# Kernel optimization log

Measured on AMD Instinct MI355X. Metric: run time of the kernel, lower is better.

## Reference

```python
import jax, jax.numpy as jnp
import numpy as np

B, M, H, E, V, U = 1024, 15, 256, 256, 30000, 1000


def setup_inputs() -> dict:
    key = jax.random.key(0)
    ks = jax.random.split(key, 24)
    s = 0.05  # weight init scale
    return {
        "input_ids": jax.random.randint(ks[0], (B, 1), 0, V),
        "input_embedding": jax.random.normal(ks[1], (B, 1, E), jnp.float32),
        "hidden": jax.random.normal(ks[2], (1, B, H), jnp.float32),
        "inter_output": jax.random.normal(ks[3], (B, M, H), jnp.float32),
        "user_list": jax.random.randint(ks[4], (B,), 0, U),
        # per-user parameter tables (torch ModuleLists of Linear); stored [in,out]
        "inter_W": jax.random.normal(ks[5], (U, H, H), jnp.float32) * s,
        "inter_b": jax.random.normal(ks[6], (U, H), jnp.float32) * s,
        "hidden_W": jax.random.normal(ks[7], (U, H, H), jnp.float32) * s,
        "hidden_b": jax.random.normal(ks[8], (U, H), jnp.float32) * s,
        "lt1_W": jax.random.normal(ks[9], (U, 2 * H, H), jnp.float32) * s,
        "lt1_b": jax.random.normal(ks[10], (U, H), jnp.float32) * s,
        "scale_W": jax.random.normal(ks[11], (U, H), jnp.float32) * s,
        "scale_b": jax.random.normal(ks[12], (U,), jnp.float32) * s,
        # GRU (1 layer), torch layout: W_ih [3H, 2E], W_hh [3H, H], gate order r,z,n
        "gru_Wih": jax.random.normal(ks[13], (3 * H, 2 * E), jnp.float32) * s,
        "gru_Whh": jax.random.normal(ks[14], (3 * H, H), jnp.float32) * s,
        "gru_bih": jax.random.normal(ks[15], (3 * H,), jnp.float32) * s,
        "gru_bhh": jax.random.normal(ks[16], (3 * H,), jnp.float32) * s,
        # output projection, stored [H, V]
        "lin_W": jax.random.normal(ks[17], (H, V), jnp.float32) * s,
        "lin_b": jax.random.normal(ks[18], (V,), jnp.float32) * s,
    }


def reference(input_ids, input_embedding, hidden, inter_output, user_list,
              inter_W, inter_b, hidden_W, hidden_b, lt1_W, lt1_b,
              scale_W, scale_b, gru_Wih, gru_Whh, gru_bih, gru_bhh,
              lin_W, lin_b):
    embedded_input = input_embedding  # dropout p=0 (eval)
    hidden_t = jnp.transpose(hidden, (1, 0, 2))  # [B,1,H]

    # per-user intra attention: gather user weights, batched GEMMs (replaces python loop)
    Wi = inter_W[user_list]                      # [B,H,H]
    inter_output_a = jnp.einsum('bmh,bho->bmo', inter_output, Wi) + inter_b[user_list][:, None, :]
    Wh = hidden_W[user_list]                     # [B,H,H]
    hidden_t_a = jnp.einsum('bih,bho->bio', hidden_t, Wh) + hidden_b[user_list][:, None, :]  # [B,1,H]
    cat = jnp.concatenate([jnp.broadcast_to(hidden_t_a, (hidden_t_a.shape[0], M, H)), inter_output_a], axis=2)  # [B,M,2H]
    result = jnp.tanh(jnp.einsum('bmk,bko->bmo', cat, lt1_W[user_list]) + lt1_b[user_list][:, None, :])  # [B,M,H]
    energies = jnp.einsum('bmh,bh->bm', result, scale_W[user_list]) + scale_b[user_list][:, None]  # [B,M]

    attn_weights = jax.nn.softmax(energies, axis=1)                      # [B,M]
    context = jnp.einsum('bm,bmh->bh', attn_weights, inter_output)[:, None, :]  # [B,1,H]

    gru_input = jnp.concatenate([embedded_input, context], axis=2)  # [B,1,2E]
    x = gru_input[:, 0, :]
    h = hidden[0]
    gi = x @ gru_Wih.T + gru_bih   # [B,3H]
    gh = h @ gru_Whh.T + gru_bhh
    gi_r, gi_z, gi_n = jnp.split(gi, 3, axis=1)
    gh_r, gh_z, gh_n = jnp.split(gh, 3, axis=1)
    r = jax.nn.sigmoid(gi_r + gh_r)
    z = jax.nn.sigmoid(gi_z + gh_z)
    n = jnp.tanh(gi_n + r * gh_n)
    h_new = (1.0 - z) * n + z * h
    gru_output = h_new[:, None, :]       # [B,1,H]
    hidden_new = h_new[None, :, :]       # [1,B,H]

    output = gru_output @ lin_W + lin_b  # [B,1,V]
    return (output, hidden_new, embedded_input, gru_output, attn_weights)
```

## Files before the change

### kernel.cpp

```cpp
#include <hip/hip_runtime.h>
#include <math.h>

#define B 1024
#define M 15
#define H 256
#define E 256
#define V 30000
#define U 1000

typedef float  vf4    __attribute__((ext_vector_type(4)));
typedef __bf16 bf16x8 __attribute__((ext_vector_type(8)));
typedef float  f32x4  __attribute__((ext_vector_type(4)));

#define O_OUT   0
#define O_HID   ((size_t)B*V)
#define O_EMB   (O_HID + (size_t)B*H)
#define O_GRU   (O_EMB + (size_t)B*E)
#define O_ATT   (O_GRU + (size_t)B*H)

#define GLDS(g, l) __builtin_amdgcn_global_load_lds( \
    (const __attribute__((address_space(1))) void*)(g), \
    (__attribute__((address_space(3))) void*)(l), 16, 0, 0)

union BF8 { __bf16 h[8]; bf16x8 v; };
union BF4 { __bf16 h[4]; unsigned long long u; };

__global__ __launch_bounds__(1024) void sort_kernel(
    const int* __restrict__ ul, int* __restrict__ order, int* __restrict__ rbase_g)
{
    __shared__ int cnt[1024];
    __shared__ int base[1024];
    const int tid = threadIdx.x;
    cnt[tid] = 0;
    __syncthreads();
    const int u = ul[tid];
    atomicAdd(&cnt[u], 1);
    __syncthreads();
    int c0 = cnt[tid];
    int v  = c0;
    for (int off = 1; off < 1024; off <<= 1) {
        int add = (tid >= off) ? cnt[tid - off] : 0;
        __syncthreads();
        v += add;
        cnt[tid] = v;
        __syncthreads();
    }
    base[tid]   = v - c0;
    rbase_g[tid] = v - c0;
    __syncthreads();
    int pos = atomicAdd(&base[u], 1);
    order[pos] = tid;
}

#define FB_ATTN 1024
#define FB_TR   500
#define FB_WC   256
#define FB_TOT  (FB_ATTN + FB_TR + FB_WC)

__global__ __launch_bounds__(256, 3) void fused_pre_kernel(
    const float* __restrict__ hidden,
    const float* __restrict__ inter_output,
    const int*   __restrict__ user_list,
    const int*   __restrict__ order,
    const int*   __restrict__ rbase,
    const float* __restrict__ inter_W,
    const float* __restrict__ inter_b,
    const float* __restrict__ hidden_W,
    const float* __restrict__ hidden_b,
    const float* __restrict__ lt1_W,
    const float* __restrict__ lt1_b,
    const float* __restrict__ scale_W,
    const float* __restrict__ scale_b,
    const float* __restrict__ emb,
    const float* __restrict__ Wih,
    const float* __restrict__ Whh,
    const float* __restrict__ lin_W,
    float* __restrict__ out,
    __bf16* __restrict__ xcat,
    __bf16* __restrict__ wcat,
    __bf16* __restrict__ WT)
{
    __shared__ __align__(16) char smem[34432];
    const int bid = blockIdx.x;
    const int tid = threadIdx.x;

    if (bid >= FB_ATTN + FB_TR) {
        const int wb   = bid - (FB_ATTN + FB_TR);
        const int wave = tid >> 6, lane = tid & 63;
        const int n    = wb * 4 + wave;
        const int r    = (n >> 2) + ((n & 3) << 8);
        #pragma unroll
        for (int i = 0; i < 3; ++i) {
            int k = i * 256 + lane * 4;
            vf4 v = {0.f, 0.f, 0.f, 0.f};
            if (r < 512) {
                v = (k < 512) ? *(const vf4*)&Wih[(size_t)r * 512 + k]
                              : *(const vf4*)&Whh[(size_t)r * 256 + (k - 512)];
            } else if (r < 768) {
                if (k < 512) v = *(const vf4*)&Wih[(size_t)r * 512 + k];
            } else {
                if (k >= 512) v = *(const vf4*)&Whh[(size_t)(r - 256) * 256 + (k - 512)];
            }
            BF4 p;
            p.h[0]=(__bf16)v[0]; p.h[1]=(__bf16)v[1]; p.h[2]=(__bf16)v[2]; p.h[3]=(__bf16)v[3];
            *(unsigned long long*)&wcat[(size_t)n * 768 + k] = p.u;
        }
        return;
    }

    if (bid >= FB_ATTN) {
        const int t   = bid - FB_ATTN;
        const int v0  = (t % 125) * 240;
        const int k0  = (t / 125) * 64;
        const int lane = tid & 63, kq = tid >> 6;
        __bf16* T = (__bf16*)smem;

        if (lane < 60) {
            #pragma unroll
            for (int i = 0; i < 4; ++i) {
                int kr = kq * 16 + i * 4;
                vf4 f0 = *(const vf4*)&lin_W[(size_t)(k0 + kr + 0) * V + v0 + lane * 4];
                vf4 f1 = *(const vf4*)&lin_W[(size_t)(k0 + kr + 1) * V + v0 + lane * 4];
                vf4 f2 = *(const vf4*)&lin_W[(size_t)(k0 + kr + 2) * V + v0 + lane * 4];
                vf4 f3 = *(const vf4*)&lin_W[(size_t)(k0 + kr + 3) * V + v0 + lane * 4];
                #pragma unroll
                for (int j = 0; j < 4; ++j) {
                    BF4 pk;
                    pk.h[0] = (__bf16)f0[j];
                    pk.h[1] = (__bf16)f1[j];
                    pk.h[2] = (__bf16)f2[j];
                    pk.h[3] = (__bf16)f3[j];
                    int v = lane * 4 + j;
                    *(unsigned long long*)&T[v * 68 + kr] = pk.u;
                }
            }
        }
        __syncthreads();
        for (int r = 0; r < 15; ++r) {
            int L = r * 256 + tid;
            int v = L >> 4, c = L & 15;
            *(unsigned long long*)&WT[(size_t)(v0 + v) * H + k0 + c * 4] =
                *(const unsigned long long*)&T[v * 68 + c * 4];
        }
        return;
    }

    const int s   = ((bid & 7) << 7) + (bid >> 3);
    const int b0  = order[s];
    const int u   = user_list[b0];

    {
        float ev = emb[(size_t)b0 * E + tid];
        float hv = hidden[(size_t)b0 * H + tid];
        xcat[(size_t)b0 * 768 + tid]       = (__bf16)ev;
        xcat[(size_t)b0 * 768 + 512 + tid] = (__bf16)hv;
        out[O_EMB + (size_t)b0 * E + tid]  = ev;
    }

    if ((s - rbase[u]) & 1) return;
    bool paired = false;
    int  b1 = b0;
    if (s + 1 < B) {
        int ob = order[s + 1];
        if (user_list[ob] == u) { paired = true; b1 = ob; }
    }

    const int lane = tid & 63;
    const int wave = tid >> 6;
    const int wn0  = wave * 64;

    __bf16* Abuf = (__bf16*)smem;
    __bf16* hta  = (__bf16*)(smem + 32768);
    float*  red  = (float*)(smem + 32768 + 1024);
    float*  e_lds= (float*)(smem + 32768 + 1024 + 512);

    {
        const int r    = tid >> 3;
        const int part = tid & 7;
        const int sm   = r >> 4;
        const int mr   = r & 15;
        const int bs   = sm ? b1 : b0;
        const bool zr  = (sm == 1) && !paired;
        #pragma unroll
        for (int it = 0; it < 8; ++it) {
            int c = part + it * 8;
            int k = c * 8;
            BF8 p;
            #pragma unroll
            for (int j = 0; j < 8; ++j) p.h[j] = (__bf16)0.f;
            if (!zr) {
                if (mr < 15 && k < 256) {
                    vf4 f0 = *(const vf4*)&inter_output[(size_t)bs * M * H + mr * H + k];
                    vf4 f1 = *(const vf4*)&inter_output[(size_t)bs * M * H + mr * H + k + 4];
                    p.h[0]=(__bf16)f0[0]; p.h[1]=(__bf16)f0[1]; p.h[2]=(__bf16)f0[2]; p.h[3]=(__bf16)f0[3];
                    p.h[4]=(__bf16)f1[0]; p.h[5]=(__bf16)f1[1]; p.h[6]=(__bf16)f1[2]; p.h[7]=(__bf16)f1[3];
                } else if (mr == 15 && k >= 256) {
                    vf4 f0 = *(const vf4*)&hidden[(size_t)bs * H + (k - 256)];
                    vf4 f1 = *(const vf4*)&hidden[(size_t)bs * H + (k - 256) + 4];
                    p.h[0]=(__bf16)f0[0]; p.h[1]=(__bf16)f0[1]; p.h[2]=(__bf16)f0[2]; p.h[3]=(__bf16)f0[3];
                    p.h[4]=(__bf16)f1[0]; p.h[5]=(__bf16)f1[1]; p.h[6]=(__bf16)f1[2]; p.h[7]=(__bf16)f1[3];
                }
            }
            *(bf16x8*)&Abuf[r * 512 + (c ^ (r & 7)) * 8] = p.v;
        }
    }
    __syncthreads();

    const float* Wi_base  = inter_W  + (size_t)u * H * H;
    const float* Wh_base  = hidden_W + (size_t)u * H * H;
    const float* lt1_base = lt1_W    + (size_t)u * 2 * H * H;

    const int ocol = wn0 + (lane & 15);
    const int krow = (lane >> 4) * 8;

    f32x4 acc1[2][4];
    #pragma unroll
    for (int mf = 0; mf < 2; ++mf)
        #pragma unroll
        for (int nf = 0; nf < 4; ++nf) { f32x4 z = {0.f,0.f,0.f,0.f}; acc1[mf][nf] = z; }

    #pragma unroll 2
    for (int ks = 0; ks < 16; ++ks) {
        const float* Bp = ((ks < 8) ? (Wi_base + (size_t)(ks * 32) * H)
                                    : (Wh_base + (size_t)((ks - 8) * 32) * H))
                          + (size_t)krow * H + ocol;
        float t[4][8];
        #pragma unroll
        for (int j = 0; j < 8; ++j)
            #pragma unroll
            for (int nf = 0; nf < 4; ++nf)
                t[nf][j] = Bp[(size_t)j * H + nf * 16];
        bf16x8 bfr[4];
        #pragma unroll
        for (int nf = 0; nf < 4; ++nf) {
            BF8 pk;
            #pragma unroll
            for (int j = 0; j < 8; ++j) pk.h[j] = (__bf16)t[nf][j];
            bfr[nf] = pk.v;
        }
        int sca = ((ks * 4 + (lane >> 4)) ^ (lane & 7)) * 8;
        bf16x8 a0 = *(const bf16x8*)&Abuf[(lane & 15) * 512 + sca];
        #pragma unroll
        for (int nf = 0; nf < 4; ++nf)
            acc1[0][nf] = __builtin_amdgcn_mfma_f32_16x16x32_bf16(a0, bfr[nf], acc1[0][nf], 0, 0, 0);
        if (paired) {
            bf16x8 a1 = *(const bf16x8*)&Abuf[(16 + (lane & 15)) * 512 + sca];
            #pragma unroll
            for (int nf = 0; nf < 4; ++nf)
                acc1[1][nf] = __builtin_amdgcn_mfma_f32_16x16x32_bf16(a1, bfr[nf], acc1[1][nf], 0, 0, 0);
        }
    }
    __syncthreads();

    if ((lane >> 4) == 3) {
        #pragma unroll
        for (int nf = 0; nf < 4; ++nf) {
            int o = wn0 + nf * 16 + (lane & 15);
            float hb = hidden_b[(size_t)u * H + o];
            hta[o]       = (__bf16)(acc1[0][nf][3] + hb);
            hta[256 + o] = (__bf16)(acc1[1][nf][3] + hb);
        }
    }
    #pragma unroll
    for (int mf = 0; mf < 2; ++mf) {
        #pragma unroll
        for (int nf = 0; nf < 4; ++nf) {
            int o  = wn0 + nf * 16 + (lane & 15);
            float bi = inter_b[(size_t)u * H + o];
            int k  = 256 + o;
            #pragma unroll
            for (int j = 0; j < 4; ++j) {
                int r  = mf * 16 + (lane >> 4) * 4 + j;
                Abuf[r * 512 + ((k >> 3) ^ (r & 7)) * 8 + (k & 7)] = (__bf16)(acc1[mf][nf][j] + bi);
            }
        }
    }
    __syncthreads();

    {
        const int r    = tid >> 3;
        const int part = tid & 7;
        const int sm   = r >> 4;
        #pragma unroll
        for (int it = 0; it < 4; ++it) {
            int c = part + it * 8;
            bf16x8 hv = *(const bf16x8*)&hta[sm * 256 + c * 8];
            *(bf16x8*)&Abuf[r * 512 + (c ^ (r & 7)) * 8] = hv;
        }
    }
    __syncthreads();

    f32x4 acc2[2][4];
    #pragma unroll
    for (int mf = 0; mf < 2; ++mf)
        #pragma unroll
        for (int nf = 0; nf < 4; ++nf) { f32x4 z = {0.f,0.f,0.f,0.f}; acc2[mf][nf] = z; }

    #pragma unroll 2
    for (int ks = 0; ks < 16; ++ks) {
        const float* Bp = lt1_base + (size_t)(ks * 32) * H + (size_t)krow * H + ocol;
        float t[4][8];
        #pragma unroll
        for (int j = 0; j < 8; ++j)
            #pragma unroll
            for (int nf = 0; nf < 4; ++nf)
                t[nf][j] = Bp[(size_t)j * H + nf * 16];
        bf16x8 bfr[4];
        #pragma unroll
        for (int nf = 0; nf < 4; ++nf) {
            BF8 pk;
            #pragma unroll
            for (int j = 0; j < 8; ++j) pk.h[j] = (__bf16)t[nf][j];
            bfr[nf] = pk.v;
        }
        int sca = ((ks * 4 + (lane >> 4)) ^ (lane & 7)) * 8;
        bf16x8 a0 = *(const bf16x8*)&Abuf[(lane & 15) * 512 + sca];
        #pragma unroll
        for (int nf = 0; nf < 4; ++nf)
            acc2[0][nf] = __builtin_amdgcn_mfma_f32_16x16x32_bf16(a0, bfr[nf], acc2[0][nf], 0, 0, 0);
        if (paired) {
            bf16x8 a1 = *(const bf16x8*)&Abuf[(16 + (lane & 15)) * 512 + sca];
            #pragma unroll
            for (int nf = 0; nf < 4; ++nf)
                acc2[1][nf] = __builtin_amdgcn_mfma_f32_16x16x32_bf16(a1, bfr[nf], acc2[1][nf], 0, 0, 0);
        }
    }

    float p0[4] = {0.f,0.f,0.f,0.f};
    float p1[4] = {0.f,0.f,0.f,0.f};
    #pragma unroll
    for (int nf = 0; nf < 4; ++nf) {
        int o = wn0 + nf * 16 + (lane & 15);
        float l1b = lt1_b[(size_t)u * H + o];
        float sw  = scale_W[(size_t)u * H + o];
        #pragma unroll
        for (int j = 0; j < 4; ++j)
            p0[j] += tanhf(acc2[0][nf][j] + l1b) * sw;
        if (paired)
            #pragma unroll
            for (int j = 0; j < 4; ++j)
                p1[j] += tanhf(acc2[1][nf][j] + l1b) * sw;
    }
    #pragma unroll
    for (int j = 0; j < 4; ++j) {
        float v = p0[j];
        v += __shfl_xor(v, 1, 64); v += __shfl_xor(v, 2, 64);
        v += __shfl_xor(v, 4, 64); v += __shfl_xor(v, 8, 64);
        if ((lane & 15) == 0) red[0 * 64 + wave * 16 + (lane >> 4) * 4 + j] = v;
        float w = p1[j];
        w += __shfl_xor(w, 1, 64); w += __shfl_xor(w, 2, 64);
        w += __shfl_xor(w, 4, 64); w += __shfl_xor(w, 8, 64);
        if ((lane & 15) == 0) red[1 * 64 + wave * 16 + (lane >> 4) * 4 + j] = w;
    }
    __syncthreads();
    if (tid < 32) {
        int sm = tid >> 4, mm = tid & 15;
        e_lds[sm * 16 + mm] = red[sm * 64 + mm] + red[sm * 64 + 16 + mm]
                            + red[sm * 64 + 32 + mm] + red[sm * 64 + 48 + mm]
                            + scale_b[u];
    }
    __syncthreads();

    const int nsm = paired ? 2 : 1;
    for (int sm = 0; sm < nsm; ++sm) {
        const int bs = sm ? b1 : b0;
        float mx = -1e30f;
        #pragma unroll
        for (int m = 0; m < M; ++m) mx = fmaxf(mx, e_lds[sm * 16 + m]);
        float sum = 0.f;
        float aw[M];
        #pragma unroll
        for (int m = 0; m < M; ++m) { aw[m] = expf(e_lds[sm * 16 + m] - mx); sum += aw[m]; }
        float inv = 1.f / sum;
        if (tid < M) out[O_ATT + (size_t)bs * M + tid] = aw[tid] * inv;
        float ctx = 0.f;
        #pragma unroll
        for (int m = 0; m < M; ++m)
            ctx += aw[m] * inter_output[(size_t)bs * M * H + m * H + tid];
        xcat[(size_t)bs * 768 + 256 + tid] = (__bf16)(ctx * inv);
    }
}

__global__ __launch_bounds__(256) void xgemm_gate_kernel(
    const __bf16* __restrict__ xcat, const __bf16* __restrict__ wcat,
    const float* __restrict__ hidden,
    const float* __restrict__ bih, const float* __restrict__ bhh,
    float* __restrict__ out, __bf16* __restrict__ hnb)
{
    const int n0   = blockIdx.x * 64;
    const int m0   = blockIdx.y * 64;
    const int tid  = threadIdx.x;
    const int wave = tid >> 6, lane = tid & 63;
    const int wm   = wave >> 1, wn = wave & 1;

    __shared__ __align__(16) __bf16 Al[64 * 128];
    __shared__ __align__(16) __bf16 Bl[64 * 128];
    __shared__ __align__(16) float  Cs[64 * 68];

    f32x4 acc[2][2];
    #pragma unroll
    for (int mf = 0; mf < 2; ++mf)
        #pragma unroll
        for (int nf = 0; nf < 2; ++nf) { f32x4 z = {0.f,0.f,0.f,0.f}; acc[mf][nf] = z; }

    for (int ks = 0; ks < 6; ++ks) {
        #pragma unroll
        for (int r = 0; r < 4; ++r) {
            int L = r * 256 + tid;
            int row = L >> 4, c = L & 15;
            int sc = c ^ (row & 7);
            GLDS(xcat + (size_t)(m0 + row) * 768 + ks * 128 + sc * 8, &Al[(size_t)L * 8]);
        }
        #pragma unroll
        for (int r = 0; r < 4; ++r) {
            int L = r * 256 + tid;
            int row = L >> 4, c = L & 15;
            int sc = c ^ (row & 7);
            GLDS(wcat + (size_t)(n0 + row) * 768 + ks * 128 + sc * 8, &Bl[(size_t)L * 8]);
        }
        __syncthreads();
        #pragma unroll
        for (int kk = 0; kk < 4; ++kk) {
            bf16x8 af[2];
            #pragma unroll
            for (int mf = 0; mf < 2; ++mf) {
                int row = wm * 32 + mf * 16 + (lane & 15);
                int c   = kk * 4 + (lane >> 4);
                af[mf] = *(const bf16x8*)&Al[row * 128 + (c ^ (row & 7)) * 8];
            }
            bf16x8 bfr[2];
            #pragma unroll
            for (int nf = 0; nf < 2; ++nf) {
                int col = wn * 32 + nf * 16 + (lane & 15);
                int c   = kk * 4 + (lane >> 4);
                bfr[nf] = *(const bf16x8*)&Bl[col * 128 + (c ^ (col & 7)) * 8];
            }
            #pragma unroll
            for (int mf = 0; mf < 2; ++mf)
                #pragma unroll
                for (int nf = 0; nf < 2; ++nf)
                    acc[mf][nf] = __builtin_amdgcn_mfma_f32_16x16x32_bf16(
                        af[mf], bfr[nf], acc[mf][nf], 0, 0, 0);
        }
        __syncthreads();
    }

    #pragma unroll
    for (int nf = 0; nf < 2; ++nf) {
        int lc = wn * 32 + nf * 16 + (lane & 15);
        #pragma unroll
        for (int mf = 0; mf < 2; ++mf) {
            int lr = wm * 32 + mf * 16 + (lane >> 4) * 4;
            f32x4 a = acc[mf][nf];
            #pragma unroll
            for (int j = 0; j < 4; ++j)
                Cs[(lr + j) * 68 + lc] = a[j];
        }
    }
    __syncthreads();

    #pragma unroll
    for (int k = 0; k < 4; ++k) {
        int idx = k * 256 + tid;
        int r = idx >> 4, g = idx & 15;
        f32x4 c = *(const f32x4*)&Cs[r * 68 + g * 4];
        int b = m0 + r;
        int j = (n0 >> 2) + g;
        float rs  = c[0] + bih[j]       + bhh[j];
        float zs  = c[1] + bih[256 + j] + bhh[256 + j];
        float gin = c[2] + bih[512 + j];
        float ghn = c[3] + bhh[512 + j];
        float h   = hidden[(size_t)b * H + j];
        float r_  = 1.f / (1.f + expf(-rs));
        float z_  = 1.f / (1.f + expf(-zs));
        float n_  = tanhf(gin + r_ * ghn);
        float hn  = (1.f - z_) * n_ + z_ * h;
        out[O_HID + (size_t)b * H + j] = hn;
        out[O_GRU + (size_t)b * H + j] = hn;
        hnb[(size_t)b * H + j] = (__bf16)hn;
    }
}

#define GBM 64
#define GBN 256
#define GBK 64
#define NTM 16
#define NWG ((117 + 1) * NTM)
__global__ __launch_bounds__(256) void out_mfma_kernel(
    const __bf16* __restrict__ hnb,
    const __bf16* __restrict__ WT,
    const float* __restrict__ lin_b,
    float* __restrict__ out)
{
    const int L  = blockIdx.x;
    const int s  = (L & 7) * (NWG / 8) + (L >> 3);
    const int nt = s >> 4, mt = s & 15;
    const int n0 = nt * GBN;
    const int m0 = mt * GBM;
    const int tid  = threadIdx.x;
    const int wave = tid >> 6, lane = tid & 63;

    __shared__ __align__(16) char gsm[GBM * H * 2 + GBN * GBK * 2];
    __bf16* Al = (__bf16*)gsm;
    __bf16* Bl = (__bf16*)(gsm + GBM * H * 2);

    #pragma unroll
    for (int r = 0; r < 8; ++r) {
        int Li = r * 256 + tid;
        int m = Li >> 5;
        int c = Li & 31;
        int sc = c ^ (m & 7);
        GLDS(hnb + (size_t)(m0 + m) * H + sc * 8, &Al[(size_t)Li * 8]);
    }

    f32x4 acc[4][4];
    #pragma unroll
    for (int mf = 0; mf < 4; ++mf)
        #pragma unroll
        for (int nf = 0; nf < 4; ++nf) {
            f32x4 z = {0.f, 0.f, 0.f, 0.f};
            acc[mf][nf] = z;
        }

    const int wn0 = wave * 64;

    for (int ks = 0; ks < 4; ++ks) {
        #pragma unroll
        for (int r = 0; r < 8; ++r) {
            int Li = r * 256 + tid;
            int n = Li >> 3;
            int c = Li & 7;
            int sc = c ^ (n & 7);
            int nn = n0 + n; if (nn >= V) nn = V - 1;
            GLDS(WT + (size_t)nn * H + ks * GBK + sc * 8, &Bl[(size_t)Li * 8]);
        }
        __syncthreads();

        #pragma unroll
        for (int kk = 0; kk < 2; ++kk) {
            bf16x8 af[4];
            #pragma unroll
            for (int mf = 0; mf < 4; ++mf) {
                int row = mf * 16 + (lane & 15);
                int c   = ks * 8 + kk * 4 + (lane >> 4);
                int cs  = c ^ (row & 7);
                af[mf] = *(const bf16x8*)&Al[row * H + cs * 8];
            }
            bf16x8 bfr[4];
            #pragma unroll
            for (int nf = 0; nf < 4; ++nf) {
                int col = wn0 + nf * 16 + (lane & 15);
                int c   = kk * 4 + (lane >> 4);
                int cs  = c ^ (col & 7);
                bfr[nf] = *(const bf16x8*)&Bl[col * GBK + cs * 8];
            }
            #pragma unroll
            for (int mf = 0; mf < 4; ++mf)
                #pragma unroll
                for (int nf = 0; nf < 4; ++nf)
                    acc[mf][nf] = __builtin_amdgcn_mfma_f32_16x16x32_bf16(
                        af[mf], bfr[nf], acc[mf][nf], 0, 0, 0);
        }
        __syncthreads();
    }

    float* Cs = (float*)gsm;
    #pragma unroll
    for (int nf = 0; nf < 4; ++nf) {
        int col = wn0 + nf * 16 + (lane & 15);
        #pragma unroll
        for (int mf = 0; mf < 4; ++mf) {
            #pragma unroll
            for (int j = 0; j < 4; ++j)
                Cs[(mf * 16 + (lane >> 4) * 4 + j) * 256 + col] = acc[mf][nf][j];
        }
    }
    __syncthreads();

    const bool nok = (n0 + lane * 4 + 3 < V);
    f32x4 lb = {0.f, 0.f, 0.f, 0.f};
    if (nok) lb = *(const f32x4*)&lin_b[n0 + lane * 4];
    for (int r = wave; r < 64; r += 4) {
        f32x4 c = *(const f32x4*)&Cs[r * 256 + lane * 4];
        c += lb;
        if (nok)
            *(f32x4*)&out[(size_t)(m0 + r) * V + n0 + lane * 4] = c;
    }
}

extern "C" void kernel_launch(void* const* d_in, const int* in_sizes, int n_in,
                              void* d_out, int out_size, void* d_ws, size_t ws_size,
                              hipStream_t stream) {
    const float* emb    = (const float*)d_in[1];
    const float* hidden = (const float*)d_in[2];
    const float* io     = (const float*)d_in[3];
    const int*   ul     = (const int*)  d_in[4];
    const float* iW     = (const float*)d_in[5];
    const float* ib     = (const float*)d_in[6];
    const float* hW     = (const float*)d_in[7];
    const float* hb     = (const float*)d_in[8];
    const float* l1W    = (const float*)d_in[9];
    const float* l1b    = (const float*)d_in[10];
    const float* sW     = (const float*)d_in[11];
    const float* sb     = (const float*)d_in[12];
    const float* Wih    = (const float*)d_in[13];
    const float* Whh    = (const float*)d_in[14];
    const float* bih    = (const float*)d_in[15];
    const float* bhh    = (const float*)d_in[16];
    const float* lW     = (const float*)d_in[17];
    const float* lb     = (const float*)d_in[18];

    float* out = (float*)d_out;
    char* ws = (char*)d_ws;
    int*    order = (int*)ws;
    int*    rbase = (int*)(ws + 4096);
    __bf16* xcat  = (__bf16*)(ws + 8192);
    __bf16* wcat  = (__bf16*)(ws + 8192 + 1572864);
    __bf16* hnb   = (__bf16*)(ws + 8192 + 2 * 1572864);
    __bf16* WT    = (__bf16*)(ws + 8192 + 2 * 1572864 + 524288);

    sort_kernel<<<1, 1024, 0, stream>>>(ul, order, rbase);
    fused_pre_kernel<<<FB_TOT, 256, 0, stream>>>(
        hidden, io, ul, order, rbase, iW, ib, hW, hb, l1W, l1b, sW, sb,
        emb, Wih, Whh, lW, out, xcat, wcat, WT);
    xgemm_gate_kernel<<<dim3(16, 16), 256, 0, stream>>>(xcat, wcat, hidden, bih, bhh, out, hnb);
    out_mfma_kernel<<<NWG, 256, 0, stream>>>(hnb, WT, lb, out);
}
```

Baseline: 240.1 us.

## Use nontemporal output stores and halve output GEMM N-tile with occupancy hint

Output writes for the logits, hidden, GRU, embedding and attention tensors, plus the transposed weight workspace, now use nontemporal stores so streaming results bypass cache retention. The output projection GEMM tile narrows from 256 to 128 columns with launch_bounds(256,3). Each block uses less LDS and registers, so more blocks can be resident, and the grid grows to 235x16 tiles. In exchange the shared A tile is reloaded by twice as many blocks, and the epilogue store pattern is rewritten for the narrower tile.

```diff
diff --git a/kernel.cpp b/kernel.cpp
--- a/kernel.cpp
+++ b/kernel.cpp
@@ -139,8 +139,9 @@
         for (int r = 0; r < 15; ++r) {
             int L = r * 256 + tid;
             int v = L >> 4, c = L & 15;
-            *(unsigned long long*)&WT[(size_t)(v0 + v) * H + k0 + c * 4] =
-                *(const unsigned long long*)&T[v * 68 + c * 4];
+            __builtin_nontemporal_store(
+                *(const unsigned long long*)&T[v * 68 + c * 4],
+                (unsigned long long*)&WT[(size_t)(v0 + v) * H + k0 + c * 4]);
         }
         return;
     }
@@ -154,7 +155,7 @@
         float hv = hidden[(size_t)b0 * H + tid];
         xcat[(size_t)b0 * 768 + tid]       = (__bf16)ev;
         xcat[(size_t)b0 * 768 + 512 + tid] = (__bf16)hv;
-        out[O_EMB + (size_t)b0 * E + tid]  = ev;
+        __builtin_nontemporal_store(ev, &out[O_EMB + (size_t)b0 * E + tid]);
     }
 
     if ((s - rbase[u]) & 1) return;
@@ -372,7 +373,8 @@
         #pragma unroll
         for (int m = 0; m < M; ++m) { aw[m] = expf(e_lds[sm * 16 + m] - mx); sum += aw[m]; }
         float inv = 1.f / sum;
-        if (tid < M) out[O_ATT + (size_t)bs * M + tid] = aw[tid] * inv;
+        if (tid < M)
+            __builtin_nontemporal_store(aw[tid] * inv, &out[O_ATT + (size_t)bs * M + tid]);
         float ctx = 0.f;
         #pragma unroll
         for (int m = 0; m < M; ++m)
@@ -475,18 +477,19 @@
         float z_  = 1.f / (1.f + expf(-zs));
         float n_  = tanhf(gin + r_ * ghn);
         float hn  = (1.f - z_) * n_ + z_ * h;
-        out[O_HID + (size_t)b * H + j] = hn;
-        out[O_GRU + (size_t)b * H + j] = hn;
+        __builtin_nontemporal_store(hn, &out[O_HID + (size_t)b * H + j]);
+        __builtin_nontemporal_store(hn, &out[O_GRU + (size_t)b * H + j]);
         hnb[(size_t)b * H + j] = (__bf16)hn;
     }
 }
 
 #define GBM 64
-#define GBN 256
+#define GBN 128
 #define GBK 64
 #define NTM 16
-#define NWG ((117 + 1) * NTM)
-__global__ __launch_bounds__(256) void out_mfma_kernel(
+#define NTN 235
+#define NWG (NTN * NTM)
+__global__ __launch_bounds__(256, 3) void out_mfma_kernel(
     const __bf16* __restrict__ hnb,
     const __bf16* __restrict__ WT,
     const float* __restrict__ lin_b,
@@ -513,20 +516,20 @@
         GLDS(hnb + (size_t)(m0 + m) * H + sc * 8, &Al[(size_t)Li * 8]);
     }
 
-    f32x4 acc[4][4];
+    f32x4 acc[4][2];
     #pragma unroll
     for (int mf = 0; mf < 4; ++mf)
         #pragma unroll
-        for (int nf = 0; nf < 4; ++nf) {
+        for (int nf = 0; nf < 2; ++nf) {
             f32x4 z = {0.f, 0.f, 0.f, 0.f};
             acc[mf][nf] = z;
         }
 
-    const int wn0 = wave * 64;
+    const int wn0 = wave * 32;
 
     for (int ks = 0; ks < 4; ++ks) {
         #pragma unroll
-        for (int r = 0; r < 8; ++r) {
+        for (int r = 0; r < 4; ++r) {
             int Li = r * 256 + tid;
             int n = Li >> 3;
             int c = Li & 7;
@@ -546,9 +549,9 @@
                 int cs  = c ^ (row & 7);
                 af[mf] = *(const bf16x8*)&Al[row * H + cs * 8];
             }
-            bf16x8 bfr[4];
-            #pragma unroll
-            for (int nf = 0; nf < 4; ++nf) {
+            bf16x8 bfr[2];
+            #pragma unroll
+            for (int nf = 0; nf < 2; ++nf) {
                 int col = wn0 + nf * 16 + (lane & 15);
                 int c   = kk * 4 + (lane >> 4);
                 int cs  = c ^ (col & 7);
@@ -557,7 +560,7 @@
             #pragma unroll
             for (int mf = 0; mf < 4; ++mf)
                 #pragma unroll
-                for (int nf = 0; nf < 4; ++nf)
+                for (int nf = 0; nf < 2; ++nf)
                     acc[mf][nf] = __builtin_amdgcn_mfma_f32_16x16x32_bf16(
                         af[mf], bfr[nf], acc[mf][nf], 0, 0, 0);
         }
@@ -566,25 +569,29 @@
 
     float* Cs = (float*)gsm;
     #pragma unroll
-    for (int nf = 0; nf < 4; ++nf) {
+    for (int nf = 0; nf < 2; ++nf) {
         int col = wn0 + nf * 16 + (lane & 15);
         #pragma unroll
         for (int mf = 0; mf < 4; ++mf) {
             #pragma unroll
             for (int j = 0; j < 4; ++j)
-                Cs[(mf * 16 + (lane >> 4) * 4 + j) * 256 + col] = acc[mf][nf][j];
-        }
-    }
-    __syncthreads();
-
-    const bool nok = (n0 + lane * 4 + 3 < V);
+                Cs[(mf * 16 + (lane >> 4) * 4 + j) * 128 + col] = acc[mf][nf][j];
+        }
+    }
+    __syncthreads();
+
+    const int c4 = tid & 31;
+    const bool nok = (n0 + c4 * 4 + 3 < V);
     f32x4 lb = {0.f, 0.f, 0.f, 0.f};
-    if (nok) lb = *(const f32x4*)&lin_b[n0 + lane * 4];
-    for (int r = wave; r < 64; r += 4) {
-        f32x4 c = *(const f32x4*)&Cs[r * 256 + lane * 4];
+    if (nok) lb = *(const f32x4*)&lin_b[n0 + c4 * 4];
+    #pragma unroll
+    for (int it = 0; it < 8; ++it) {
+        int idx = it * 256 + tid;
+        int r = idx >> 5;
+        f32x4 c = *(const f32x4*)&Cs[r * 128 + c4 * 4];
         c += lb;
         if (nok)
-            *(f32x4*)&out[(size_t)(m0 + r) * V + n0 + lane * 4] = c;
+            __builtin_nontemporal_store(c, (f32x4*)&out[(size_t)(m0 + r) * V + n0 + c4 * 4]);
     }
 }
 
```

Result: faster. 232.5 us (-3.1%).
